# Optimization experiments

Measured on AMD Instinct MI355X. Metric: run time of the kernel, lower is better.

## Reference

```python
import jax, jax.numpy as jnp
import numpy as np

B, N, DIM = 4, 2048, 1024
HEADS, DH = 16, 64
INNER = HEADS * DH
SCALE = 8.0
EPS = 1e-5


def setup_inputs() -> dict:
    key = jax.random.key(0)
    ks = jax.random.split(key, 8)
    x = jax.random.normal(ks[0], (B, N, DIM), dtype=jnp.float32)
    context_mask = jax.random.bernoulli(ks[1], 0.9, (B, N))
    gamma = jnp.ones((DIM,), dtype=jnp.float32)
    null_kv = jax.random.normal(ks[2], (2, HEADS, 1, DH), dtype=jnp.float32)
    Wq = jax.random.normal(ks[3], (DIM, INNER), dtype=jnp.float32) * 0.02
    Wkv = jax.random.normal(ks[4], (DIM, 2 * INNER), dtype=jnp.float32) * 0.02
    # q_scale init: scale / dim_head**-0.5 = 8 * sqrt(64) = 64
    q_scale = jnp.full((DH,), SCALE * (DH ** 0.5), dtype=jnp.float32)
    k_scale = jnp.ones((DH,), dtype=jnp.float32)
    Wout = jax.random.normal(ks[5], (INNER, DIM), dtype=jnp.float32) * 0.02
    return {"x": x, "context_mask": context_mask, "gamma": gamma,
            "null_kv": null_kv, "Wq": Wq, "Wkv": Wkv,
            "q_scale": q_scale, "k_scale": k_scale, "Wout": Wout}


def _l2norm(t):
    return t / jnp.sqrt(jnp.sum(t * t, axis=-1, keepdims=True) + 1e-12)


def reference(x, context_mask, gamma, null_kv, Wq, Wkv, q_scale, k_scale, Wout):
    b, n, _ = x.shape
    # LayerNorm (beta buffer is zeros)
    mu = jnp.mean(x, axis=-1, keepdims=True)
    var = jnp.mean((x - mu) ** 2, axis=-1, keepdims=True)
    xn = (x - mu) / jnp.sqrt(var + EPS) * gamma
    # projections
    q = (xn @ Wq).reshape(b, n, HEADS, DH)
    kv = xn @ Wkv
    k = kv[..., :INNER].reshape(b, n, HEADS, DH)
    v = kv[..., INNER:].reshape(b, n, HEADS, DH)
    # null kv token: [h,1,d] -> [b,1,h,d]
    nk = jnp.broadcast_to(null_kv[0].transpose(1, 0, 2)[None], (b, 1, HEADS, DH))
    nv = jnp.broadcast_to(null_kv[1].transpose(1, 0, 2)[None], (b, 1, HEADS, DH))
    k = jnp.concatenate([nk, k], axis=1)  # [b, n+1, h, d]
    v = jnp.concatenate([nv, v], axis=1)
    # cosine-sim attention with learned per-dim scales
    q = _l2norm(q) * q_scale
    k = _l2norm(k) * k_scale
    # bias from mask (padded True for null token)
    mask = jnp.pad(context_mask, ((0, 0), (1, 0)), constant_values=True)
    bias = jnp.where(mask, 0.0, -10000.0)[:, None, None, :]  # [b,1,1,n+1]
    # memory_efficient_attention applies 1/sqrt(dh) internally
    scores = jnp.einsum('bqhd,bkhd->bhqk', q, k) * (DH ** -0.5) + bias
    attn = jax.nn.softmax(scores, axis=-1)
    out = jnp.einsum('bhqk,bkhd->bqhd', attn, v).reshape(b, n, INNER)
    return out @ Wout
```

## Files before the change

### kernel.cpp

```cpp
#include <hip/hip_runtime.h>
#include <hip/hip_bf16.h>
#include <stdint.h>


using f32x4  = __attribute__((ext_vector_type(4))) float;
using bf16x8 = __attribute__((ext_vector_type(8))) __bf16;
using f16x8  = __attribute__((ext_vector_type(8))) _Float16;
using uintv4 = __attribute__((ext_vector_type(4))) unsigned int;

__device__ __forceinline__ unsigned short f2b(float f) {
    unsigned u = __float_as_uint(f);
    u += 0x7fffu + ((u >> 16) & 1u);
    return (unsigned short)(u >> 16);
}
__device__ __forceinline__ unsigned short f2h(float f) {
    return __builtin_bit_cast(unsigned short, (_Float16)f);
}
__device__ __forceinline__ f32x4 mfma16(bf16x8 a, bf16x8 b, f32x4 c) {
    return __builtin_amdgcn_mfma_f32_16x16x32_bf16(a, b, c, 0, 0, 0);
}
__device__ __forceinline__ f32x4 mfma16h(f16x8 a, f16x8 b, f32x4 c) {
    return __builtin_amdgcn_mfma_f32_16x16x32_f16(a, b, c, 0, 0, 0);
}
__device__ __forceinline__ unsigned pk16(float a, float b) {
    return __builtin_bit_cast(unsigned, __builtin_amdgcn_cvt_pkrtz(a, b));
}
__device__ __forceinline__ void gl_lds16(const void* g, void* l) {
    __builtin_amdgcn_global_load_lds(
        (const __attribute__((address_space(1))) unsigned int*)g,
        (__attribute__((address_space(3))) unsigned int*)l, 16, 0, 0);
}

__global__ __launch_bounds__(256) void transpose_f2b(
    const float* __restrict__ in, unsigned short* __restrict__ out,
    int R, int C)
{
    __shared__ unsigned short t[32][33];
    int tx = threadIdx.x, ty = threadIdx.y;
    int c = blockIdx.x * 32 + tx;
#pragma unroll
    for (int i = 0; i < 4; ++i) {
        int r = blockIdx.y * 32 + ty + i * 8;
        t[ty + i * 8][tx] = f2b(in[(size_t)r * C + c]);
    }
    __syncthreads();
    int r2 = blockIdx.y * 32 + tx;
#pragma unroll
    for (int i = 0; i < 4; ++i) {
        int c2 = blockIdx.x * 32 + ty + i * 8;
        out[(size_t)c2 * R + r2] = t[tx][ty + i * 8];
    }
}

__global__ __launch_bounds__(256) void ln_kernel(
    const float* __restrict__ x, const float* __restrict__ gamma,
    unsigned short* __restrict__ xn)
{
    int row = blockIdx.x, tid = threadIdx.x;
    int wave = tid >> 6, lane = tid & 63;
    float4 raw = *(const float4*)(x + ((size_t)row << 10) + (tid << 2));
    float v[4] = { raw.x, raw.y, raw.z, raw.w };
    float s  = v[0] + v[1] + v[2] + v[3];
    float s2 = v[0]*v[0] + v[1]*v[1] + v[2]*v[2] + v[3]*v[3];
#pragma unroll
    for (int off = 1; off < 64; off <<= 1) {
        s  += __shfl_xor(s, off);
        s2 += __shfl_xor(s2, off);
    }
    __shared__ float ps[4], ps2[4], sh[2];
    if (lane == 0) { ps[wave] = s; ps2[wave] = s2; }
    __syncthreads();
    if (tid == 0) {
        float S  = ps[0] + ps[1] + ps[2] + ps[3];
        float S2 = ps2[0] + ps2[1] + ps2[2] + ps2[3];
        float mu  = S * (1.f / 1024.f);
        float var = S2 * (1.f / 1024.f) - mu * mu;
        sh[0] = mu; sh[1] = rsqrtf(var + 1e-5f);
    }
    __syncthreads();
    float mu = sh[0], rstd = sh[1];
    float4 g4 = *(const float4*)(gamma + (tid << 2));
    float g[4] = { g4.x, g4.y, g4.z, g4.w };
    unsigned short o[4];
#pragma unroll
    for (int i = 0; i < 4; ++i) o[i] = f2b((v[i] - mu) * rstd * g[i]);
    uint2 out;
    out.x = (unsigned)o[0] | ((unsigned)o[1] << 16);
    out.y = (unsigned)o[2] | ((unsigned)o[3] << 16);
    *(uint2*)(xn + ((size_t)row << 10) + (tid << 2)) = out;
}

template<int MODE>
__global__ __launch_bounds__(256, 2) void gemm_bt(
    const unsigned short* __restrict__ A,
    const unsigned short* __restrict__ Bt,
    void* __restrict__ C0,
    unsigned short* __restrict__ Ck,
    unsigned short* __restrict__ Vout,
    const float* __restrict__ qs, const float* __restrict__ ks,
    int K)
{
    __shared__ __align__(16) unsigned char smem[32768];
    __bf16* As = (__bf16*)smem;
    __bf16* Bs = (__bf16*)(smem + 16384);

    int tid = threadIdx.x, lane = tid & 63, wave = tid >> 6;
    int quad = lane >> 4, l15 = lane & 15;
    int m0 = blockIdx.y * 128, n0 = blockIdx.x * 128;
    int wm = (wave & 1) * 64, wn = (wave >> 1) * 64;
    f32x4 acc[4][4] = {};

    const int srow8 = lane >> 3;
    const int w7    = lane & 7;
    const int swz   = ((w7 ^ srow8) << 3);
    const unsigned short* gA = A  + (size_t)(m0 + wave * 32 + srow8) * K + swz;
    const unsigned short* gB = Bt + (size_t)(n0 + wave * 32 + srow8) * K + swz;
    const size_t r8 = (size_t)8 * K;

    const int nsteps = K >> 6;
    for (int s = 0; s < nsteps; ++s) {
#pragma unroll
        for (int p = 0; p < 4; ++p)
            gl_lds16(gA + p * r8, &As[(wave * 32 + p * 8) * 64]);
#pragma unroll
        for (int p = 0; p < 4; ++p)
            gl_lds16(gB + p * r8, &Bs[(wave * 32 + p * 8) * 64]);
        gA += 64; gB += 64;
        __syncthreads();
#pragma unroll
        for (int kk = 0; kk < 2; ++kk) {
            bf16x8 af[4], bfv[4];
#pragma unroll
            for (int i = 0; i < 4; ++i) {
                int row = wm + i * 16 + l15;
                int g = ((kk << 2) + quad) ^ (l15 & 7);
                af[i] = *(const bf16x8*)&As[row * 64 + (g << 3)];
            }
#pragma unroll
            for (int j = 0; j < 4; ++j) {
                int row = wn + j * 16 + l15;
                int g = ((kk << 2) + quad) ^ (l15 & 7);
                bfv[j] = *(const bf16x8*)&Bs[row * 64 + (g << 3)];
            }
#pragma unroll
            for (int i = 0; i < 4; ++i)
#pragma unroll
                for (int j = 0; j < 4; ++j)
                    acc[i][j] = mfma16(af[i], bfv[j], acc[i][j]);
        }
        __syncthreads();
    }

    if (MODE == 2) {
#pragma unroll
        for (int i = 0; i < 4; ++i)
#pragma unroll
            for (int j = 0; j < 4; ++j) {
                int row = m0 + wm + i * 16 + quad * 4;
                int col = n0 + wn + j * 16 + l15;
                size_t base = (size_t)row * 1024 + col;
#pragma unroll
                for (int r = 0; r < 4; ++r)
                    ((float*)C0)[base + (size_t)r * 1024] = acc[i][j][r];
            }
        return;
    }

    if (n0 >= 2048) {
        unsigned short* tileL = (unsigned short*)smem + wave * 4096;
        int hv = (n0 + wn - 2048) >> 6;
        int bidx = m0 >> 11;
        int tok0w = (m0 + wm) & 2047;
        size_t vbase = (size_t)((((bidx << 4) + hv) << 6)) * 2056;
#pragma unroll
        for (int i = 0; i < 4; ++i)
#pragma unroll
            for (int j = 0; j < 4; ++j) {
                int d = j * 16 + l15;
                int tk = (i * 16 + quad * 4) ^ ((d & 7) << 3);
                unsigned u01 = (unsigned)f2h(acc[i][j][0])
                             | ((unsigned)f2h(acc[i][j][1]) << 16);
                unsigned u23 = (unsigned)f2h(acc[i][j][2])
                             | ((unsigned)f2h(acc[i][j][3]) << 16);
                *(unsigned*)&tileL[d * 64 + tk]     = u01;
                *(unsigned*)&tileL[d * 64 + tk + 2] = u23;
            }
#pragma unroll
        for (int rr = 0; rr < 16; ++rr) {
            int d = rr * 4 + quad;
            uint2 val = *(const uint2*)
                &tileL[d * 64 + ((l15 * 4) ^ ((d & 7) << 3))];
            *(uint2*)(Vout + vbase + (size_t)d * 2056 + tok0w + l15 * 4) = val;
        }
        return;
    }

    const bool isQ = (n0 < 1024);
    float sc[4];
#pragma unroll
    for (int j = 0; j < 4; ++j) {
        float s = isQ ? qs[j * 16 + l15] : ks[j * 16 + l15];
        sc[j] = isQ ? s * (0.125f * 1.44269504088896f) : s;
    }
    unsigned short* outp = isQ ? (unsigned short*)C0 : Ck;
    const int coln0 = isQ ? n0 : (n0 - 1024);
#pragma unroll
    for (int i = 0; i < 4; ++i)
#pragma unroll
        for (int r = 0; r < 4; ++r) {
            float ss = 0.f;
#pragma unroll
            for (int j = 0; j < 4; ++j) ss += acc[i][j][r] * acc[i][j][r];
            ss += __shfl_xor(ss, 1); ss += __shfl_xor(ss, 2);
            ss += __shfl_xor(ss, 4); ss += __shfl_xor(ss, 8);
            float mul = rsqrtf(ss + 1e-12f);
            size_t rowbase = (size_t)(m0 + wm + i * 16 + quad * 4 + r) * 1024
                           + coln0 + wn + l15;
#pragma unroll
            for (int j = 0; j < 4; ++j) {
                float v = acc[i][j][r];
                outp[rowbase + j * 16] = f2b(v * mul * sc[j]);
            }
        }
}

__global__ __launch_bounds__(256) void nullkv_kernel(
    const float* __restrict__ null_kv, const float* __restrict__ k_scale,
    unsigned short* __restrict__ knull, unsigned short* __restrict__ Vt)
{
    int wave = threadIdx.x >> 6, lane = threadIdx.x & 63;
    int h = blockIdx.x * 4 + wave;
    int idx = (h << 6) + lane;
    float kvl = null_kv[idx];
    float ss = kvl * kvl;
#pragma unroll
    for (int off = 1; off < 64; off <<= 1) ss += __shfl_xor(ss, off);
    knull[idx] = f2b(kvl * rsqrtf(ss + 1e-12f) * k_scale[lane]);
    unsigned short vn = f2h(null_kv[1024 + idx]);
#pragma unroll
    for (int b = 0; b < 4; ++b)
        Vt[((size_t)(((b << 4) + h) << 6) + lane) * 2056 + 2048] = vn;
    int t = blockIdx.x * 256 + threadIdx.x;
#pragma unroll
    for (int rr = 0; rr < 4; ++rr) {
        size_t row = (size_t)t * 4 + rr;
#pragma unroll
        for (int c = 0; c < 7; ++c)
            Vt[row * 2056 + 2049 + c] = 0;
    }
}

__global__ __launch_bounds__(256, 4) void attn_kernel(
    const unsigned short* __restrict__ qn,
    const unsigned short* __restrict__ kvK,
    const unsigned short* __restrict__ knull,
    const unsigned short* __restrict__ Vt,
    const int* __restrict__ mask,
    unsigned short* __restrict__ ao)
{
    __shared__ __bf16    Kt[2][64 * 64];
    __shared__ _Float16  Vl[2][64 * 64];
    __shared__ __align__(16) float biasLds[2][64];

    const int tid = threadIdx.x, lane = tid & 63, wave = tid >> 6;
    const int quad = lane >> 4, l15 = lane & 15;
    const int bh = blockIdx.x;
    const int b = bh >> 4, h = bh & 15;
    const int mbase = blockIdx.y * 128 + wave * 32;
    const size_t rowoff = (size_t)b * 2048;

    bf16x8 qf[2][2];
#pragma unroll
    for (int rg = 0; rg < 2; ++rg)
#pragma unroll
        for (int ks = 0; ks < 2; ++ks)
            qf[rg][ks] = *(const bf16x8*)
                &qn[((rowoff + mbase + rg * 16 + l15) << 10) + (h << 6) + ks * 32 + quad * 8];

    const int t8  = lane >> 3;
    const int w7  = lane & 7;
    const int ksc = (w7 ^ t8) << 3;
    const size_t vrow0 = ((size_t)bh << 6);

    const int r0v = wave * 16 + t8;
    const int r1v = wave * 16 + 8 + t8;
    auto Tof = [](int r) {
        return ((r >> 5) << 5) | (((r >> 2) & 3) << 3)
             | (((r >> 4) & 1) << 2) | (r & 3);
    };
    const int T0 = Tof(r0v), T1 = Tof(r1v);

    const unsigned short* kp0 = kvK + ((rowoff + T0) << 10) + (h << 6) + ksc;
    const unsigned short* kp1 = kvK + ((rowoff + T1) << 10) + (h << 6) + ksc;
    const unsigned short* vp0 = Vt + (vrow0 + r0v) * 2056 + ((w7 ^ t8) << 3);
    const unsigned short* vp1 = Vt + (vrow0 + r1v) * 2056 + ((w7 ^ t8) << 3);

    auto issueFast = [&](int bf) {
        gl_lds16(kp0, &Kt[bf][(wave * 16) * 64]);
        gl_lds16(kp1, &Kt[bf][(wave * 16 + 8) * 64]);
        gl_lds16(vp0, &Vl[bf][(wave * 16) * 64]);
        gl_lds16(vp1, &Vl[bf][(wave * 16 + 8) * 64]);
        kp0 += 65536; kp1 += 65536;
        vp0 += 64; vp1 += 64;
    };
    auto issue32 = [&](int bf) {
        const unsigned short* kc =
            kvK + ((rowoff + 2047) << 10) + (h << 6) + ksc;
        const unsigned short* s0 = (T0 == 0) ? knull + (h << 6) + ksc : kc;
        gl_lds16(s0, &Kt[bf][(wave * 16) * 64]);
        gl_lds16(kc, &Kt[bf][(wave * 16 + 8) * 64]);
        gl_lds16(Vt + (vrow0 + r0v) * 2056 + 2048, &Vl[bf][(wave * 16) * 64]);
        gl_lds16(Vt + (vrow0 + r1v) * 2056 + 2048, &Vl[bf][(wave * 16 + 8) * 64]);
    };
    auto biasFor = [&](int nt) -> float {
        int j = (nt << 6) + lane;
        float bv = -512.f;
        if (j < 2048) { if (mask[(b << 11) + j] != 0) bv = 0.f; }
        else if (j == 2048) bv = 0.f;
        return bv;
    };

    const uintv4 onesu = { 0x3c003c00u, 0x3c003c00u, 0x3c003c00u, 0x3c003c00u };
    const f16x8 ones = __builtin_bit_cast(f16x8, onesu);

    f32x4 O[2][4] = {};
    f32x4 rsacc[2] = {};

    issueFast(0);
    float bcur = 0.f;
    if (wave == 0) bcur = biasFor(0);

    for (int nt = 0; nt < 33; ++nt) {
        const int buf = nt & 1;
        if (wave == 0) biasLds[buf][lane] = bcur;
        __syncthreads();
        if (nt < 31) {
            issueFast(buf ^ 1);
            if (wave == 0) bcur = biasFor(nt + 1);
        } else if (nt == 31) {
            issue32(buf ^ 1);
            if (wave == 0) bcur = biasFor(32);
        }

#pragma unroll
        for (int g = 0; g < 2; ++g) {
            float4 b0 = *(const float4*)&biasLds[buf][(g << 5) + (quad << 3)];
            float4 b1 = *(const float4*)&biasLds[buf][(g << 5) + (quad << 3) + 4];
            f32x4 s[2][2];
#pragma unroll
            for (int rg = 0; rg < 2; ++rg) {
                s[rg][0] = f32x4{ b0.x, b0.y, b0.z, b0.w };
                s[rg][1] = f32x4{ b1.x, b1.y, b1.z, b1.w };
            }
#pragma unroll
            for (int t = 0; t < 2; ++t) {
                const __bf16* kb = &Kt[buf][((g * 2 + t) * 16 + l15) * 64];
                bf16x8 k0 = *(const bf16x8*)&kb[(quad ^ (l15 & 7)) << 3];
                bf16x8 k1 = *(const bf16x8*)&kb[((4 + quad) ^ (l15 & 7)) << 3];
#pragma unroll
                for (int rg = 0; rg < 2; ++rg) {
                    s[rg][t] = mfma16(k0, qf[rg][0], s[rg][t]);
                    s[rg][t] = mfma16(k1, qf[rg][1], s[rg][t]);
                }
            }
            f16x8 vf8[4];
#pragma unroll
            for (int dt = 0; dt < 4; ++dt)
                vf8[dt] = *(const f16x8*)
                    &Vl[buf][(dt * 16 + l15) * 64
                             + ((((g << 2) + quad) ^ (l15 & 7)) << 3)];
#pragma unroll
            for (int rg = 0; rg < 2; ++rg) {
                float e0 = __builtin_amdgcn_exp2f(s[rg][0][0]);
                float e1 = __builtin_amdgcn_exp2f(s[rg][0][1]);
                float e2 = __builtin_amdgcn_exp2f(s[rg][0][2]);
                float e3 = __builtin_amdgcn_exp2f(s[rg][0][3]);
                float e4 = __builtin_amdgcn_exp2f(s[rg][1][0]);
                float e5 = __builtin_amdgcn_exp2f(s[rg][1][1]);
                float e6 = __builtin_amdgcn_exp2f(s[rg][1][2]);
                float e7 = __builtin_amdgcn_exp2f(s[rg][1][3]);
                uintv4 pu = { pk16(e0, e1), pk16(e2, e3),
                              pk16(e4, e5), pk16(e6, e7) };
                f16x8 p = __builtin_bit_cast(f16x8, pu);
                rsacc[rg] = mfma16h(p, ones, rsacc[rg]);
#pragma unroll
                for (int dt = 0; dt < 4; ++dt)
                    O[rg][dt] = mfma16h(p, vf8[dt], O[rg][dt]);
            }
        }
    }

#pragma unroll
    for (int rg = 0; rg < 2; ++rg) {
        float inv[4];
#pragma unroll
        for (int r = 0; r < 4; ++r) inv[r] = 1.f / rsacc[rg][r];
#pragma unroll
        for (int dt = 0; dt < 4; ++dt) {
            size_t base = ((rowoff + mbase + rg * 16 + quad * 4) << 10)
                        + (h << 6) + dt * 16 + l15;
#pragma unroll
            for (int r = 0; r < 4; ++r)
                ao[base + ((size_t)r << 10)] = f2b(O[rg][dt][r] * inv[r]);
        }
    }
}

extern "C" void kernel_launch(void* const* d_in, const int* in_sizes, int n_in,
                              void* d_out, int out_size, void* d_ws, size_t ws_size,
                              hipStream_t stream)
{
    const float* x       = (const float*)d_in[0];
    const int*   mask    = (const int*)d_in[1];
    const float* gamma   = (const float*)d_in[2];
    const float* null_kv = (const float*)d_in[3];
    const float* Wq      = (const float*)d_in[4];
    const float* Wkv     = (const float*)d_in[5];
    const float* q_scale = (const float*)d_in[6];
    const float* k_scale = (const float*)d_in[7];
    const float* Wout    = (const float*)d_in[8];

    char* ws = (char*)d_ws;
    const size_t VTG_OFF   = (size_t)48u << 20;
    const size_t VTG_SIZE  = (size_t)4096 * 4112;
    const size_t WQKV_OFF  = VTG_OFF + VTG_SIZE;
    const size_t WQKV_SIZE = (size_t)3072 * 1024 * 2;
    unsigned short* xn    = (unsigned short*)(ws);
    unsigned short* ao    = xn;
    unsigned short* q     = (unsigned short*)(ws + ((size_t)16u << 20));
    unsigned short* WoutT = q;
    unsigned short* kvK   = (unsigned short*)(ws + ((size_t)32u << 20));
    unsigned short* VtG   = (unsigned short*)(ws + VTG_OFF);
    unsigned short* WqkvT = (unsigned short*)(ws + WQKV_OFF);
    unsigned short* knull = (unsigned short*)(ws + WQKV_OFF + WQKV_SIZE);

    dim3 tb(32, 8);
    transpose_f2b<<<dim3(32, 32), tb, 0, stream>>>(Wq,  WqkvT,             1024, 1024);
    transpose_f2b<<<dim3(64, 32), tb, 0, stream>>>(Wkv, WqkvT + (1u << 20), 1024, 2048);

    ln_kernel<<<8192, 256, 0, stream>>>(x, gamma, xn);

    nullkv_kernel<<<4, 256, 0, stream>>>(null_kv, k_scale, knull, VtG);

    gemm_bt<0><<<dim3(24, 64), 256, 0, stream>>>(xn, WqkvT, q, kvK, VtG,
                                                 q_scale, k_scale, 1024);

    attn_kernel<<<dim3(64, 16), 256, 0, stream>>>(q, kvK, knull, VtG, mask, ao);

    transpose_f2b<<<dim3(32, 32), tb, 0, stream>>>(Wout, WoutT, 1024, 1024);

    gemm_bt<2><<<dim3(8, 64), 256, 0, stream>>>(ao, WoutT, d_out, nullptr, nullptr,
                                                nullptr, nullptr, 1024);
}
```

Measured before the change: 289.5 us.

## Double-buffer GEMM LDS tiles and remap the grid to a 1D block order

The bf16 GEMM now keeps two 64-wide K slices in LDS, 64 KB in total. It issues the global-to-LDS loads for the next slice before running the MFMAs on the current one, which drops one barrier per step and overlaps memory with compute. The launch grid becomes 1D, with each group of 8 consecutive blocks sharing an M row inside the Q, K or V segment, to improve cache reuse of the A tiles. The larger LDS footprint could limit occupancy. Correctness depends on the one remaining barrier making sure the async loads have finished.

```diff
diff --git a/kernel.cpp b/kernel.cpp
--- a/kernel.cpp
+++ b/kernel.cpp
@@ -100,13 +100,17 @@
     const float* __restrict__ qs, const float* __restrict__ ks,
     int K)
 {
-    __shared__ __align__(16) unsigned char smem[32768];
+    __shared__ __align__(16) unsigned char smem[65536];
     __bf16* As = (__bf16*)smem;
-    __bf16* Bs = (__bf16*)(smem + 16384);
+    __bf16* Bs = (__bf16*)(smem + 32768);
 
     int tid = threadIdx.x, lane = tid & 63, wave = tid >> 6;
     int quad = lane >> 4, l15 = lane & 15;
-    int m0 = blockIdx.y * 128, n0 = blockIdx.x * 128;
+    const int bid = blockIdx.x;
+    const int role = bid >> 9;
+    const int rr_  = bid & 511;
+    int m0 = (rr_ >> 3) * 128;
+    int n0 = role * 1024 + (rr_ & 7) * 128;
     int wm = (wave & 1) * 64, wn = (wave >> 1) * 64;
     f32x4 acc[4][4] = {};
 
@@ -117,16 +121,26 @@
     const unsigned short* gB = Bt + (size_t)(n0 + wave * 32 + srow8) * K + swz;
     const size_t r8 = (size_t)8 * K;
 
+    auto stage = [&](int bf) {
+        __bf16* Ab = As + bf * 8192;
+        __bf16* Bb = Bs + bf * 8192;
+#pragma unroll
+        for (int p = 0; p < 4; ++p)
+            gl_lds16(gA + p * r8, &Ab[(wave * 32 + p * 8) * 64]);
+#pragma unroll
+        for (int p = 0; p < 4; ++p)
+            gl_lds16(gB + p * r8, &Bb[(wave * 32 + p * 8) * 64]);
+        gA += 64; gB += 64;
+    };
+
+    stage(0);
+    __syncthreads();
     const int nsteps = K >> 6;
     for (int s = 0; s < nsteps; ++s) {
-#pragma unroll
-        for (int p = 0; p < 4; ++p)
-            gl_lds16(gA + p * r8, &As[(wave * 32 + p * 8) * 64]);
-#pragma unroll
-        for (int p = 0; p < 4; ++p)
-            gl_lds16(gB + p * r8, &Bs[(wave * 32 + p * 8) * 64]);
-        gA += 64; gB += 64;
-        __syncthreads();
+        const int cur = s & 1;
+        if (s + 1 < nsteps) stage(cur ^ 1);
+        const __bf16* Ab = As + cur * 8192;
+        const __bf16* Bb = Bs + cur * 8192;
 #pragma unroll
         for (int kk = 0; kk < 2; ++kk) {
             bf16x8 af[4], bfv[4];
@@ -134,13 +148,13 @@
             for (int i = 0; i < 4; ++i) {
                 int row = wm + i * 16 + l15;
                 int g = ((kk << 2) + quad) ^ (l15 & 7);
-                af[i] = *(const bf16x8*)&As[row * 64 + (g << 3)];
+                af[i] = *(const bf16x8*)&Ab[row * 64 + (g << 3)];
             }
 #pragma unroll
             for (int j = 0; j < 4; ++j) {
                 int row = wn + j * 16 + l15;
                 int g = ((kk << 2) + quad) ^ (l15 & 7);
-                bfv[j] = *(const bf16x8*)&Bs[row * 64 + (g << 3)];
+                bfv[j] = *(const bf16x8*)&Bb[row * 64 + (g << 3)];
             }
 #pragma unroll
             for (int i = 0; i < 4; ++i)
@@ -186,8 +200,8 @@
                 *(unsigned*)&tileL[d * 64 + tk + 2] = u23;
             }
 #pragma unroll
-        for (int rr = 0; rr < 16; ++rr) {
-            int d = rr * 4 + quad;
+        for (int rrr = 0; rrr < 16; ++rrr) {
+            int d = rrr * 4 + quad;
             uint2 val = *(const uint2*)
                 &tileL[d * 64 + ((l15 * 4) ^ ((d & 7) << 3))];
             *(uint2*)(Vout + vbase + (size_t)d * 2056 + tok0w + l15 * 4) = val;
@@ -435,20 +449,20 @@
     unsigned short* knull = (unsigned short*)(ws + WQKV_OFF + WQKV_SIZE);
 
     dim3 tb(32, 8);
-    transpose_f2b<<<dim3(32, 32), tb, 0, stream>>>(Wq,  WqkvT,             1024, 1024);
+    transpose_f2b<<<dim3(32, 32), tb, 0, stream>>>(Wq,  WqkvT,              1024, 1024);
     transpose_f2b<<<dim3(64, 32), tb, 0, stream>>>(Wkv, WqkvT + (1u << 20), 1024, 2048);
 
     ln_kernel<<<8192, 256, 0, stream>>>(x, gamma, xn);
 
     nullkv_kernel<<<4, 256, 0, stream>>>(null_kv, k_scale, knull, VtG);
 
-    gemm_bt<0><<<dim3(24, 64), 256, 0, stream>>>(xn, WqkvT, q, kvK, VtG,
-                                                 q_scale, k_scale, 1024);
+    gemm_bt<0><<<dim3(1536), 256, 0, stream>>>(xn, WqkvT, q, kvK, VtG,
+                                               q_scale, k_scale, 1024);
 
     attn_kernel<<<dim3(64, 16), 256, 0, stream>>>(q, kvK, knull, VtG, mask, ao);
 
     transpose_f2b<<<dim3(32, 32), tb, 0, stream>>>(Wout, WoutT, 1024, 1024);
 
-    gemm_bt<2><<<dim3(8, 64), 256, 0, stream>>>(ao, WoutT, d_out, nullptr, nullptr,
-                                                nullptr, nullptr, 1024);
-}
+    gemm_bt<2><<<dim3(512), 256, 0, stream>>>(ao, WoutT, d_out, nullptr, nullptr,
+                                              nullptr, nullptr, 1024);
+}
```

After: 286.2 us. No clear change (-1.1%).
